# Kernel tuning notes

Hardware: AMD Instinct MI355X
Metric: run time of the kernel (lower is better)

Reference implementation:

```python
import jax, jax.numpy as jnp
import numpy as np
from jax import lax

B, IC, OC = 1, 16, 32
K, STRIDE, PAD, DIL = 3, 1, 1, 1
D = 32  # each of the 4 spatial dims


def setup_inputs() -> dict:
    key = jax.random.key(0)
    k1, k2, k3 = jax.random.split(key, 3)
    inputs = jax.random.normal(k1, (B, IC, D, D, D, D), dtype=jnp.float32)
    weight = jax.random.normal(k2, (OC, IC * K ** 4), dtype=jnp.float32)
    bias = jax.random.normal(k3, (1, OC, 1, 1, 1, 1), dtype=jnp.float32)
    return {"inputs": inputs, "weight": weight, "bias": bias}


def _conv4d(x, w_flat):
    # x: [B, IC, D1, D2, D3, D4]; w_flat: [OC, IC*K^4]
    b, c, d1, d2, d3, d4 = x.shape
    w = w_flat.reshape(OC, c, K, K, K, K)
    o1 = (d1 + 2 * PAD - DIL * (K - 1) - 1) // STRIDE + 1
    # pad only the first spatial dim; 3D conv handles the rest
    xp = jnp.pad(x, ((0, 0), (0, 0), (PAD, PAD), (0, 0), (0, 0), (0, 0)))
    out = None
    for ki in range(K):  # small fixed loop over first kernel dim
        start = ki * DIL
        xs = lax.slice_in_dim(xp, start, start + (o1 - 1) * STRIDE + 1, stride=STRIDE, axis=2)
        # [B, C, O1, D2, D3, D4] -> fold O1 into batch for a 3D conv
        xb = xs.transpose(0, 2, 1, 3, 4, 5).reshape(b * o1, c, d2, d3, d4)
        y = lax.conv_general_dilated(
            xb, w[:, :, ki],
            window_strides=(STRIDE,) * 3,
            padding=[(PAD, PAD)] * 3,
            rhs_dilation=(DIL,) * 3,
            dimension_numbers=("NCDHW", "OIDHW", "NCDHW"))
        out = y if out is None else out + y
    _, _, o2, o3, o4 = out.shape
    out = out.reshape(b, o1, OC, o2, o3, o4).transpose(0, 2, 1, 3, 4, 5)
    return out  # [B, OC, O1, O2, O3, O4]


def reference(inputs, weight, bias):
    return _conv4d(inputs, weight) + bias
```

## Files before the change

### kernel.cpp

```cpp
#include <hip/hip_runtime.h>
#include <hip/hip_bf16.h>
#include <stdint.h>


typedef __bf16 bf16x8 __attribute__((ext_vector_type(8)));
typedef float f32x16 __attribute__((ext_vector_type(16)));

#define X_IC_STRIDE 1048576
#define W_K 1296
#define WPACK_DWORDS 23040
#define XPACK_OFF 98304
#define XPACK_BYTES 33554432u
#define ZOFF XPACK_BYTES
#define H_SLOTS 1632
#define H_BYTES 26624
#define LEGACY_LDS 52224

__device__ __forceinline__ unsigned rne_bf16(float f) {
    unsigned b = __builtin_bit_cast(unsigned, f);
    return (b + 0x7FFFu + ((b >> 16) & 1u)) >> 16;
}

__device__ __forceinline__ void gload_lds16(const unsigned char* g, unsigned char* s) {
    __builtin_amdgcn_global_load_lds(
        (const __attribute__((address_space(1))) unsigned int*)g,
        (__attribute__((address_space(3))) unsigned int*)s, 16, 0, 0);
}

__device__ __forceinline__ void fence_sched() { __builtin_amdgcn_sched_barrier(0); }

__device__ __forceinline__ void pack_w_body(int D, const float* __restrict__ w,
                                            unsigned* __restrict__ wpack) {
    if (D >= WPACK_DWORDS) return;
    int t    = D & 3;
    int lane = (D >> 2) & 63;
    int fi   = D >> 8;
    int p    = fi % 5;
    int dadb = (fi / 5) % 9;
    int g    = fi / 45;
    int kh   = lane >> 5;
    int oc   = lane & 31;
    int slot = 2 * p + kh;
    unsigned pk = 0u;
    if (slot < 9) {
        int da = dadb / 3, db = dadb % 3;
        int dc = slot / 3, dd = slot % 3;
        int koff = da * 27 + db * 9 + dc * 3 + dd;
        int ic0  = g * 8 + 2 * t;
        unsigned lo = rne_bf16(w[oc * W_K + ic0 * 81 + koff]);
        unsigned hi = rne_bf16(w[oc * W_K + (ic0 + 1) * 81 + koff]);
        pk = lo | (hi << 16);
    }
    wpack[D] = pk;
}

__global__ void pack_w_kernel(const float* __restrict__ w, unsigned* __restrict__ wpack) {
    pack_w_body(blockIdx.x * 256 + threadIdx.x, w, wpack);
}

__global__ __launch_bounds__(256) void pack_xw_kernel(const float* __restrict__ x,
                                                      const float* __restrict__ w,
                                                      unsigned char* __restrict__ xpack,
                                                      unsigned* __restrict__ wpack) {
    const int bid = blockIdx.x;
    const int tid = threadIdx.x;
    if (bid < (WPACK_DWORDS + 255) / 256)
        pack_w_body(bid * 256 + tid, w, wpack);

    const unsigned P0 = (unsigned)(bid * 256 + tid) * 2u;
    float2 v[16];
#pragma unroll
    for (int ic = 0; ic < 16; ++ic)
        v[ic] = *(const float2*)(x + (size_t)ic * X_IC_STRIDE + P0);

    uint4 o[4];
#pragma unroll
    for (int pt = 0; pt < 2; ++pt) {
        unsigned u[16];
#pragma unroll
        for (int ic = 0; ic < 16; ++ic)
            u[ic] = rne_bf16(pt ? v[ic].y : v[ic].x);
        o[pt * 2]     = make_uint4(u[0] | (u[1] << 16),  u[2] | (u[3] << 16),
                                   u[4] | (u[5] << 16),  u[6] | (u[7] << 16));
        o[pt * 2 + 1] = make_uint4(u[8] | (u[9] << 16),  u[10] | (u[11] << 16),
                                   u[12] | (u[13] << 16), u[14] | (u[15] << 16));
    }
#pragma unroll
    for (int j = 0; j < 4; ++j)
        *(uint4*)(xpack + (size_t)P0 * 32 + j * 16) = o[j];

    if (P0 == 0) {
        *(uint4*)(xpack + ZOFF) = make_uint4(0u, 0u, 0u, 0u);
        *(uint4*)(xpack + ZOFF + 16) = make_uint4(0u, 0u, 0u, 0u);
    }
}

__global__ __launch_bounds__(256, 3) void conv4d_pipe(
    const unsigned char* __restrict__ wpack,
    const unsigned char* __restrict__ xpack,
    const float* __restrict__ bias,
    float* __restrict__ out)
{
    __shared__ __attribute__((aligned(16))) unsigned char ldsH0[H_BYTES];
    __shared__ __attribute__((aligned(16))) unsigned char ldsH1[H_BYTES];

    const int tid  = threadIdx.x;
    const int lane = tid & 63;
    const int wv   = tid >> 6;
    const int kh   = lane >> 5;
    const int ln   = lane & 31;

    const int bid = blockIdx.x;
    const int blk = ((bid & 7) << 8) | (bid >> 3);
    const int c0  = (blk & 7) * 4;
    const int b0  = ((blk >> 3) & 15) * 2;
    const int a0  = (blk >> 7) * 2;
    const int ai  = wv >> 1, bi = wv & 1;

    int pbase[3];
#pragma unroll
    for (int p = 0; p < 3; ++p) {
        int slot = 2 * p + kh;
        int dc = slot / 3, dd = slot % 3;
        pbase[p] = dc * 544 + (ln + dd) * 16;
    }

    const int nld   = (wv < 2) ? 7 : 6;
    const int sbase = (wv < 2) ? wv * 448 : 896 + (wv - 2) * 384;

    unsigned xoffH[2][7];
#pragma unroll
    for (int h = 0; h < 2; ++h)
#pragma unroll
        for (int i = 0; i < 7; ++i) {
            int s   = sbase + i * 64 + lane;
            int row = h * 48 + s / 34;
            int dpr = s % 34;
            int rc = row % 6; int r2 = row / 6;
            int rb = r2 & 3;  int ra = r2 >> 2;
            int a_in = a0 + ra - 1, b_in = b0 + rb - 1;
            int c_in = c0 + rc - 1, d_in = dpr - 1;
            bool v = (s < H_SLOTS) &
                     ((unsigned)a_in < 32u) & ((unsigned)b_in < 32u) &
                     ((unsigned)c_in < 32u) & ((unsigned)d_in < 32u);
            unsigned P = (unsigned)(((a_in * 32 + b_in) * 32 + c_in) * 32 + d_in);
            xoffH[h][i] = v ? P * 32u : ZOFF;
        }

    f32x16 acc[4];
#pragma unroll
    for (int ci = 0; ci < 4; ++ci)
#pragma unroll
        for (int r = 0; r < 16; ++r) acc[ci][r] = 0.f;

    bf16x8 af[5];

    auto stage_half = [&](unsigned char* dstArr, int h, int g) {
        const unsigned gofs = (unsigned)(g << 4);
        unsigned char* base = dstArr + (sbase << 4);
#pragma unroll
        for (int i = 0; i < 7; ++i) {
            if (i < 6 || wv < 2) {
                if (i < nld)
                    gload_lds16(xpack + xoffH[h][i] + gofs, base + ((i * 64) << 4));
            }
        }
    };

    auto cstep = [&](int g, int da) {
        const int ca = ai + da;
        const unsigned char* hb = ((ca & 2) ? ldsH1 : ldsH0) + (ca & 1) * 13056;
#pragma unroll
        for (int db = 0; db < 3; ++db) {
            const int fi  = g * 9 + da * 3 + db;
            const int nfi = (fi + 1 > 17) ? 17 : fi + 1;
            bf16x8 afn[5];
#pragma unroll
            for (int p = 0; p < 5; ++p)
                afn[p] = *(const bf16x8*)(wpack + ((size_t)nfi * 5 + p) * 1024 + lane * 16);

            const unsigned char* rbase = hb + (bi + db) * 3264;
            __builtin_amdgcn_s_setprio(1);
#pragma unroll
            for (int p = 0; p < 2; ++p) {
                const unsigned char* bp = rbase + pbase[p];
                bf16x8 f6[6];
#pragma unroll
                for (int j = 0; j < 6; ++j)
                    f6[j] = *(const bf16x8*)(bp + j * 544);
#pragma unroll
                for (int ci = 0; ci < 4; ++ci)
                    acc[ci] = __builtin_amdgcn_mfma_f32_32x32x16_bf16(
                        af[p], f6[ci], acc[ci], 0, 0, 0);
#pragma unroll
                for (int ci = 0; ci < 4; ++ci)
                    acc[ci] = __builtin_amdgcn_mfma_f32_32x32x16_bf16(
                        af[p + 3], f6[ci + 2], acc[ci], 0, 0, 0);
            }
            {
                const unsigned char* bp = rbase + pbase[2];
#pragma unroll
                for (int ci = 0; ci < 4; ++ci) {
                    bf16x8 bfrag = *(const bf16x8*)(bp + ci * 544);
                    acc[ci] = __builtin_amdgcn_mfma_f32_32x32x16_bf16(
                        af[2], bfrag, acc[ci], 0, 0, 0);
                }
            }
            __builtin_amdgcn_s_setprio(0);
#pragma unroll
            for (int p = 0; p < 5; ++p) af[p] = afn[p];
        }
    };

    stage_half(ldsH0, 0, 0);
    stage_half(ldsH1, 1, 0);
#pragma unroll
    for (int p = 0; p < 5; ++p)
        af[p] = *(const bf16x8*)(wpack + (size_t)p * 1024 + lane * 16);
    __syncthreads();

    cstep(0, 0);
    cstep(0, 1);
    __syncthreads();

    stage_half(ldsH0, 0, 1);
    fence_sched();
    cstep(0, 2);
    __syncthreads();

    stage_half(ldsH1, 1, 1);
    fence_sched();
    cstep(1, 0);
    __syncthreads();

    cstep(1, 1);
    cstep(1, 2);

    float bv[16];
#pragma unroll
    for (int r = 0; r < 16; ++r) bv[r] = bias[(r & 3) + 8 * (r >> 2) + 4 * kh];

    const size_t sp_base = (((size_t)(a0 + ai) * 32 + (b0 + bi)) * 32 + c0);
#pragma unroll
    for (int ci = 0; ci < 4; ++ci) {
#pragma unroll
        for (int r = 0; r < 16; ++r) {
            int oc_ = (r & 3) + 8 * (r >> 2) + 4 * kh;
            out[(size_t)oc_ * X_IC_STRIDE + (sp_base + ci) * 32 + ln] = acc[ci][r] + bv[r];
        }
    }
}

__global__ __launch_bounds__(256, 3) void conv4d_legacy(
    const float* __restrict__ x,
    const unsigned char* __restrict__ wpack,
    const float* __restrict__ bias,
    float* __restrict__ out)
{
    __shared__ __attribute__((aligned(16))) unsigned char lds[LEGACY_LDS];

    const int tid  = threadIdx.x;
    const int lane = tid & 63;
    const int wv   = tid >> 6;
    const int kh   = lane >> 5;
    const int ln   = lane & 31;

    const int bid = blockIdx.x;
    const int blk = ((bid & 7) << 8) | (bid >> 3);
    const int c0  = (blk & 7) * 4;
    const int b0  = ((blk >> 3) & 15) * 2;
    const int a0  = (blk >> 7) * 2;
    const int ai  = wv >> 1, bi = wv & 1;

    int pbase[3];
#pragma unroll
    for (int p = 0; p < 3; ++p) {
        int slot = 2 * p + kh;
        int dc = slot / 3, dd = slot % 3;
        pbase[p] = dc * 544 + (ln + dd) * 16;
    }

    f32x16 acc[4];
#pragma unroll
    for (int ci = 0; ci < 4; ++ci)
#pragma unroll
        for (int r = 0; r < 16; ++r) acc[ci][r] = 0.f;

    bf16x8 af[5];
#pragma unroll
    for (int p = 0; p < 5; ++p)
        af[p] = *(const bf16x8*)(wpack + (size_t)p * 1024 + lane * 16);

    for (int g = 0; g < 2; ++g) {
        if (g) __syncthreads();
        for (int t = tid; t < 96 * 34; t += 256) {
            int dpr = t % 34;
            int row = t / 34;
            int rc = row % 6; int r2 = row / 6;
            int rb = r2 & 3;  int ra = r2 >> 2;
            int a_in = a0 + ra - 1, b_in = b0 + rb - 1;
            int c_in = c0 + rc - 1, d_in = dpr - 1;
            uint4 pk = make_uint4(0u, 0u, 0u, 0u);
            if ((unsigned)a_in < 32u && (unsigned)b_in < 32u &&
                (unsigned)c_in < 32u && (unsigned)d_in < 32u) {
                const float* xp = x + (size_t)(g * 8) * X_IC_STRIDE +
                                  (((a_in * 32 + b_in) * 32 + c_in) * 32 + d_in);
                unsigned u[8];
#pragma unroll
                for (int j = 0; j < 8; ++j)
                    u[j] = rne_bf16(xp[j * X_IC_STRIDE]);
                pk.x = u[0] | (u[1] << 16); pk.y = u[2] | (u[3] << 16);
                pk.z = u[4] | (u[5] << 16); pk.w = u[6] | (u[7] << 16);
            }
            *(uint4*)(lds + t * 16) = pk;
        }
        __syncthreads();

        for (int dadb = 0; dadb < 9; ++dadb) {
            const int fi  = g * 9 + dadb;
            const int nfi = (fi + 1 > 17) ? 17 : fi + 1;
            bf16x8 afn[5];
#pragma unroll
            for (int p = 0; p < 5; ++p)
                afn[p] = *(const bf16x8*)(wpack + ((size_t)nfi * 5 + p) * 1024 + lane * 16);

            const int da = dadb / 3, db = dadb % 3;
            const int ubase = ((ai + da) * 24 + (bi + db) * 6) * 544;
#pragma unroll
            for (int p = 0; p < 2; ++p) {
                const unsigned char* bp = lds + ubase + pbase[p];
                bf16x8 f6[6];
#pragma unroll
                for (int j = 0; j < 6; ++j)
                    f6[j] = *(const bf16x8*)(bp + j * 544);
#pragma unroll
                for (int ci = 0; ci < 4; ++ci)
                    acc[ci] = __builtin_amdgcn_mfma_f32_32x32x16_bf16(
                        af[p], f6[ci], acc[ci], 0, 0, 0);
#pragma unroll
                for (int ci = 0; ci < 4; ++ci)
                    acc[ci] = __builtin_amdgcn_mfma_f32_32x32x16_bf16(
                        af[p + 3], f6[ci + 2], acc[ci], 0, 0, 0);
            }
            {
                const unsigned char* bp = lds + ubase + pbase[2];
#pragma unroll
                for (int ci = 0; ci < 4; ++ci) {
                    bf16x8 bfrag = *(const bf16x8*)(bp + ci * 544);
                    acc[ci] = __builtin_amdgcn_mfma_f32_32x32x16_bf16(
                        af[2], bfrag, acc[ci], 0, 0, 0);
                }
            }
#pragma unroll
            for (int p = 0; p < 5; ++p) af[p] = afn[p];
        }
    }

    float bv[16];
#pragma unroll
    for (int r = 0; r < 16; ++r) bv[r] = bias[(r & 3) + 8 * (r >> 2) + 4 * kh];

    const size_t sp_base = (((size_t)(a0 + ai) * 32 + (b0 + bi)) * 32 + c0);
#pragma unroll
    for (int ci = 0; ci < 4; ++ci) {
#pragma unroll
        for (int r = 0; r < 16; ++r) {
            int oc_ = (r & 3) + 8 * (r >> 2) + 4 * kh;
            out[(size_t)oc_ * X_IC_STRIDE + (sp_base + ci) * 32 + ln] = acc[ci][r] + bv[r];
        }
    }
}

extern "C" void kernel_launch(void* const* d_in, const int* in_sizes, int n_in,
                              void* d_out, int out_size, void* d_ws, size_t ws_size,
                              hipStream_t stream) {
    const float* x    = (const float*)d_in[0];
    const float* w    = (const float*)d_in[1];
    const float* bias = (const float*)d_in[2];
    float* out        = (float*)d_out;
    unsigned* wpack   = (unsigned*)d_ws;
    unsigned char* xpack = (unsigned char*)d_ws + XPACK_OFF;

    if (ws_size >= (size_t)XPACK_OFF + XPACK_BYTES + 32) {
        pack_xw_kernel<<<dim3(2048), dim3(256), 0, stream>>>(x, w, xpack, wpack);
        conv4d_pipe<<<dim3(2048), dim3(256), 0, stream>>>(
            (const unsigned char*)d_ws, xpack, bias, out);
    } else {
        pack_w_kernel<<<dim3((WPACK_DWORDS + 255) / 256), dim3(256), 0, stream>>>(w, wpack);
        conv4d_legacy<<<dim3(2048), dim3(256), 0, stream>>>(
            x, (const unsigned char*)d_ws, bias, out);
    }
}
```

Baseline: 259.2 us.

## Replace two-half LDS staging with a three-slot quarter ring buffer

Input tiles are now staged in LDS as three 13 KB quarter slices used as a rotating ring, instead of two 26 KB halves. The compute steps are reordered, and each step prefetches the weight fragments the next step needs, so loading the next slice overlaps with MFMA work on the others. The smaller LDS footprint allows launch bounds of 4 blocks per CU instead of 3, to raise occupancy. The cost is more barriers, and register pressure at 4 waves per SIMD could cause spills, since the kernel holds large accumulators and weight fragments.

```diff
diff --git a/kernel.cpp b/kernel.cpp
--- a/kernel.cpp
+++ b/kernel.cpp
@@ -12,8 +12,8 @@
 #define XPACK_OFF 98304
 #define XPACK_BYTES 33554432u
 #define ZOFF XPACK_BYTES
-#define H_SLOTS 1632
-#define H_BYTES 26624
+#define Q_SLOTS 816
+#define Q_BYTES 13312
 #define LEGACY_LDS 52224
 
 __device__ __forceinline__ unsigned rne_bf16(float f) {
@@ -95,14 +95,15 @@
     }
 }
 
-__global__ __launch_bounds__(256, 3) void conv4d_pipe(
+__global__ __launch_bounds__(256, 4) void conv4d_ring(
     const unsigned char* __restrict__ wpack,
     const unsigned char* __restrict__ xpack,
     const float* __restrict__ bias,
     float* __restrict__ out)
 {
-    __shared__ __attribute__((aligned(16))) unsigned char ldsH0[H_BYTES];
-    __shared__ __attribute__((aligned(16))) unsigned char ldsH1[H_BYTES];
+    __shared__ __attribute__((aligned(16))) unsigned char sA[Q_BYTES];
+    __shared__ __attribute__((aligned(16))) unsigned char sB[Q_BYTES];
+    __shared__ __attribute__((aligned(16))) unsigned char sC[Q_BYTES];
 
     const int tid  = threadIdx.x;
     const int lane = tid & 63;
@@ -125,26 +126,22 @@
         pbase[p] = dc * 544 + (ln + dd) * 16;
     }
 
-    const int nld   = (wv < 2) ? 7 : 6;
-    const int sbase = (wv < 2) ? wv * 448 : 896 + (wv - 2) * 384;
-
-    unsigned xoffH[2][7];
-#pragma unroll
-    for (int h = 0; h < 2; ++h)
-#pragma unroll
-        for (int i = 0; i < 7; ++i) {
-            int s   = sbase + i * 64 + lane;
-            int row = h * 48 + s / 34;
+    unsigned xoffQ[4][4];
+#pragma unroll
+    for (int q = 0; q < 4; ++q)
+#pragma unroll
+        for (int i = 0; i < 4; ++i) {
+            int s   = wv * 256 + i * 64 + lane;
+            int r24 = s / 34;
             int dpr = s % 34;
-            int rc = row % 6; int r2 = row / 6;
-            int rb = r2 & 3;  int ra = r2 >> 2;
-            int a_in = a0 + ra - 1, b_in = b0 + rb - 1;
+            int rb = r24 / 6, rc = r24 % 6;
+            int a_in = a0 + q - 1, b_in = b0 + rb - 1;
             int c_in = c0 + rc - 1, d_in = dpr - 1;
-            bool v = (s < H_SLOTS) &
+            bool v = (s < Q_SLOTS) &
                      ((unsigned)a_in < 32u) & ((unsigned)b_in < 32u) &
                      ((unsigned)c_in < 32u) & ((unsigned)d_in < 32u);
             unsigned P = (unsigned)(((a_in * 32 + b_in) * 32 + c_in) * 32 + d_in);
-            xoffH[h][i] = v ? P * 32u : ZOFF;
+            xoffQ[q][i] = v ? P * 32u : ZOFF;
         }
 
     f32x16 acc[4];
@@ -155,31 +152,27 @@
 
     bf16x8 af[5];
 
-    auto stage_half = [&](unsigned char* dstArr, int h, int g) {
+    auto stage_q = [&](unsigned char* dst, int q, int g) {
         const unsigned gofs = (unsigned)(g << 4);
-        unsigned char* base = dstArr + (sbase << 4);
-#pragma unroll
-        for (int i = 0; i < 7; ++i) {
-            if (i < 6 || wv < 2) {
-                if (i < nld)
-                    gload_lds16(xpack + xoffH[h][i] + gofs, base + ((i * 64) << 4));
-            }
+        unsigned char* base = dst + (wv << 12);
+#pragma unroll
+        for (int i = 0; i < 4; ++i) {
+            if (i == 0 || wv < 3)
+                gload_lds16(xpack + xoffQ[q][i] + gofs, base + (i << 10));
         }
     };
 
-    auto cstep = [&](int g, int da) {
-        const int ca = ai + da;
-        const unsigned char* hb = ((ca & 2) ? ldsH1 : ldsH0) + (ca & 1) * 13056;
+    auto cstep = [&](const unsigned char* qb, int fiBase, int nextBase) {
 #pragma unroll
         for (int db = 0; db < 3; ++db) {
-            const int fi  = g * 9 + da * 3 + db;
-            const int nfi = (fi + 1 > 17) ? 17 : fi + 1;
+            const int fi  = fiBase + db;
+            const int nfi = (db < 2) ? fi + 1 : nextBase;
             bf16x8 afn[5];
 #pragma unroll
             for (int p = 0; p < 5; ++p)
                 afn[p] = *(const bf16x8*)(wpack + ((size_t)nfi * 5 + p) * 1024 + lane * 16);
 
-            const unsigned char* rbase = hb + (bi + db) * 3264;
+            const unsigned char* rbase = qb + (bi + db) * 3264;
             __builtin_amdgcn_s_setprio(1);
 #pragma unroll
             for (int p = 0; p < 2; ++p) {
@@ -212,29 +205,35 @@
         }
     };
 
-    stage_half(ldsH0, 0, 0);
-    stage_half(ldsH1, 1, 0);
+    stage_q(sA, 0, 0);
+    stage_q(sB, 1, 0);
+    stage_q(sC, 2, 0);
 #pragma unroll
     for (int p = 0; p < 5; ++p)
         af[p] = *(const bf16x8*)(wpack + (size_t)p * 1024 + lane * 16);
     __syncthreads();
 
-    cstep(0, 0);
-    cstep(0, 1);
-    __syncthreads();
-
-    stage_half(ldsH0, 0, 1);
+    cstep(ai ? sB : sA, 0, 3);
+    __syncthreads();
+    stage_q(sA, 3, 0);
     fence_sched();
-    cstep(0, 2);
-    __syncthreads();
-
-    stage_half(ldsH1, 1, 1);
+    cstep(ai ? sC : sB, 3, 6);
+    __syncthreads();
+    stage_q(sB, 2, 1);
     fence_sched();
-    cstep(1, 0);
-    __syncthreads();
-
-    cstep(1, 1);
-    cstep(1, 2);
+    cstep(ai ? sA : sC, 6, 15);
+    __syncthreads();
+    stage_q(sC, 3, 1);
+    __syncthreads();
+    stage_q(sA, 1, 1);
+    fence_sched();
+    cstep(ai ? sC : sB, 15, 12);
+    __syncthreads();
+    stage_q(sC, 0, 1);
+    fence_sched();
+    cstep(ai ? sB : sA, 12, 9);
+    __syncthreads();
+    cstep(ai ? sA : sC, 9, 0);
 
     float bv[16];
 #pragma unroll
@@ -383,7 +382,7 @@
 
     if (ws_size >= (size_t)XPACK_OFF + XPACK_BYTES + 32) {
         pack_xw_kernel<<<dim3(2048), dim3(256), 0, stream>>>(x, w, xpack, wpack);
-        conv4d_pipe<<<dim3(2048), dim3(256), 0, stream>>>(
+        conv4d_ring<<<dim3(2048), dim3(256), 0, stream>>>(
             (const unsigned char*)d_ws, xpack, bias, out);
     } else {
         pack_w_kernel<<<dim3((WPACK_DWORDS + 255) / 256), dim3(256), 0, stream>>>(w, wpack);
```

Result: slower. 291.7 us (+12.5%).
